# Kernel tuning notes

Measured on AMD Instinct MI355X. Metric: run time of the kernel, lower is better.

Reference implementation:

```python
import jax, jax.numpy as jnp
import numpy as np

B, S, H = 32, 1024, 512  # batch, src_len, hidden_dim


def setup_inputs() -> dict:
    key = jax.random.key(0)
    k1, k2, k3, k4, k5 = jax.random.split(key, 5)
    hidden = jax.random.normal(k1, (B, H), dtype=jnp.float32)
    encoder_outputs = jax.random.normal(k2, (B, S, 2 * H), dtype=jnp.float32)
    # nn.Linear(3H, H): weight stored here as [3H, H] (input-major) with bias [H]
    W = jax.random.normal(k3, (3 * H, H), dtype=jnp.float32) / np.sqrt(3 * H)
    b = jax.random.normal(k4, (H,), dtype=jnp.float32) * 0.01
    v = jax.random.normal(k5, (H,), dtype=jnp.float32) / np.sqrt(H)
    return {"hidden": hidden, "encoder_outputs": encoder_outputs, "W": W, "b": b, "v": v}


def reference(hidden, encoder_outputs, W, b, v):
    # concat((repeat(hidden), encoder_outputs)) @ W  ==  hidden @ W[:H] (broadcast) + enc @ W[H:]
    Wh, We = W[:H], W[H:]                         # [H,H], [2H,H]
    h_proj = hidden @ Wh                           # [B,H]
    e_proj = jnp.einsum('bse,eh->bsh', encoder_outputs, We)  # [B,S,H]
    energy = jnp.tanh(h_proj[:, None, :] + e_proj + b)       # [B,S,H]
    # bmm(v[B,1,H], energy^T[B,H,S]) -> scores [B,S]
    scores = jnp.einsum('bsh,h->bs', energy, v)
    return jax.nn.softmax(scores, axis=1)
```

## Files before the change

### kernel.cpp

```cpp
#include <hip/hip_runtime.h>
#include <math.h>

#define B_ 32
#define S_ 1024
#define H_ 512
#define K_ 1024
#define M_ (B_ * S_)

typedef __attribute__((ext_vector_type(8))) short bf16x8;
typedef __attribute__((ext_vector_type(4))) float f32x4;

__device__ __forceinline__ void split_bf16(float f, unsigned short& hi, unsigned short& lo) {
    unsigned u = __float_as_uint(f);
    unsigned rh = (u + 0x7fffu + ((u >> 16) & 1u)) >> 16;
    hi = (unsigned short)rh;
    float fh = __uint_as_float(rh << 16);
    float r = f - fh;
    unsigned ur = __float_as_uint(r);
    unsigned rl = (ur + 0x7fffu + ((ur >> 16) & 1u)) >> 16;
    lo = (unsigned short)rl;
}

__device__ __forceinline__ void split8_store(const float4& x, const float4& y,
                                             unsigned short* hiP, unsigned short* loP) {
    union { unsigned short us[8]; uint4 u; } h, l;
    split_bf16(x.x, h.us[0], l.us[0]);
    split_bf16(x.y, h.us[1], l.us[1]);
    split_bf16(x.z, h.us[2], l.us[2]);
    split_bf16(x.w, h.us[3], l.us[3]);
    split_bf16(y.x, h.us[4], l.us[4]);
    split_bf16(y.y, h.us[5], l.us[5]);
    split_bf16(y.z, h.us[6], l.us[6]);
    split_bf16(y.w, h.us[7], l.us[7]);
    *reinterpret_cast<uint4*>(hiP) = h.u;
    *reinterpret_cast<uint4*>(loP) = l.u;
}

__device__ __forceinline__ void async_copy16(const void* g, void* l) {
    __builtin_amdgcn_global_load_lds(
        (const __attribute__((address_space(1))) void*)g,
        (__attribute__((address_space(3))) void*)l, 16, 0, 0);
}

__global__ __launch_bounds__(256) void prep_kernel(
    const float* __restrict__ hidden, const float* __restrict__ W,
    const float* __restrict__ bias, float* __restrict__ hb,
    unsigned short* __restrict__ Wh, unsigned short* __restrict__ Wl)
{
    __shared__ float red[4][64];
    __shared__ float t[32][33];
    const int bx = blockIdx.x;
    if (bx < 256) {
        const int tid = threadIdx.x;
        const int h0  = (bx & 7) * 64;
        const int b   = bx >> 3;
        const int h   = h0 + (tid & 63);
        const int ks  = tid >> 6;
        const float* hrow = hidden + b * H_;
        float acc = 0.f;
        #pragma unroll 8
        for (int k = ks * 128; k < ks * 128 + 128; ++k)
            acc = fmaf(hrow[k], W[(size_t)k * H_ + h], acc);
        red[ks][tid & 63] = acc;
        __syncthreads();
        if (tid < 64)
            hb[b * H_ + h0 + tid] = red[0][tid] + red[1][tid] + red[2][tid]
                                  + red[3][tid] + bias[h0 + tid];
    } else {
        const float* We = W + (size_t)H_ * H_;
        const int cx = bx - 256;
        const int k0 = (cx & 31) * 32, n0 = (cx >> 5) * 32;
        const int tx = threadIdx.x & 31, ty = threadIdx.x >> 5;
        #pragma unroll
        for (int j = 0; j < 4; ++j) {
            const int k = ty + 8 * j;
            t[k][tx] = We[(size_t)(k0 + k) * H_ + n0 + tx];
        }
        __syncthreads();
        #pragma unroll
        for (int j = 0; j < 4; ++j) {
            const int n = ty + 8 * j;
            unsigned short hi, lo;
            split_bf16(t[tx][n], hi, lo);
            Wh[(size_t)(n0 + n) * K_ + k0 + tx] = hi;
            Wl[(size_t)(n0 + n) * K_ + k0 + tx] = lo;
        }
    }
}

__global__ __launch_bounds__(256, 2) void gemm_fused(
    const float* __restrict__ EO,
    const unsigned short* __restrict__ Bth,
    const unsigned short* __restrict__ Btl,
    const float* __restrict__ hb, const float* __restrict__ v,
    float* __restrict__ partial)
{
    __shared__ unsigned short ldsA[2][2][4096];
    __shared__ unsigned short ldsB[2][2][4096];

    const int tid  = threadIdx.x;
    const int nt   = blockIdx.x;
    const int mt   = blockIdx.y;
    const int row0 = mt * 128;
    const int col0 = nt * 128;
    const int batch = row0 >> 10;

    const int lane   = tid & 63;
    const int wave   = tid >> 6;
    const int wm     = wave >> 1, wn = wave & 1;
    const int lanelo = lane & 15, quad = lane >> 4;

    size_t gaA[2];
    int offA[2];
    #pragma unroll
    for (int s = 0; s < 2; ++s) {
        const int seg = tid + 256 * s;
        const int m = seg >> 2, sg = seg & 3;
        gaA[s] = (size_t)(row0 + m) * K_ + sg * 8;
        offA[s] = m * 32 + (sg ^ ((m >> 1) & 3)) * 8;
    }
    size_t gb[2];
    int offB[2];
    #pragma unroll
    for (int j = 0; j < 2; ++j) {
        const int iss = wave * 2 + j;
        const int r   = iss * 16 + (lane >> 2);
        const int qg  = (lane & 3) ^ ((r >> 1) & 3);
        gb[j] = (size_t)(col0 + r) * K_ + qg * 8;
        offB[j] = iss * 512;
    }

    f32x4 acc[4][4];
    #pragma unroll
    for (int i = 0; i < 4; ++i)
        #pragma unroll
        for (int j = 0; j < 4; ++j)
            acc[i][j] = (f32x4){0.f, 0.f, 0.f, 0.f};

    float4 a0[2], a1[2];
    #pragma unroll
    for (int s = 0; s < 2; ++s) {
        a0[s] = *reinterpret_cast<const float4*>(EO + gaA[s]);
        a1[s] = *reinterpret_cast<const float4*>(EO + gaA[s] + 4);
    }
    #pragma unroll
    for (int j = 0; j < 2; ++j) {
        async_copy16(Bth + gb[j], &ldsB[0][0][offB[j]]);
        async_copy16(Btl + gb[j], &ldsB[0][1][offB[j]]);
    }
    #pragma unroll
    for (int s = 0; s < 2; ++s)
        split8_store(a0[s], a1[s], &ldsA[0][0][offA[s]], &ldsA[0][1][offA[s]]);

    for (int i = 0; i < 32; ++i) {
        __syncthreads();
        const int cur = i & 1, nxt = cur ^ 1;
        const int k0n = 32 * (i + 1);
        if (i < 31) {
            #pragma unroll
            for (int s = 0; s < 2; ++s) {
                a0[s] = *reinterpret_cast<const float4*>(EO + gaA[s] + k0n);
                a1[s] = *reinterpret_cast<const float4*>(EO + gaA[s] + k0n + 4);
            }
            #pragma unroll
            for (int j = 0; j < 2; ++j) {
                async_copy16(Bth + gb[j] + k0n, &ldsB[nxt][0][offB[j]]);
                async_copy16(Btl + gb[j] + k0n, &ldsB[nxt][1][offB[j]]);
            }
        }

        bf16x8 a_h[4], a_l[4], b_h[4], b_l[4];
        #pragma unroll
        for (int fi = 0; fi < 4; ++fi) {
            const int m  = wm * 64 + fi * 16 + lanelo;
            const int sa = quad ^ ((m >> 1) & 3);
            a_h[fi] = *reinterpret_cast<const bf16x8*>(&ldsA[cur][0][m * 32 + sa * 8]);
            a_l[fi] = *reinterpret_cast<const bf16x8*>(&ldsA[cur][1][m * 32 + sa * 8]);
            const int n  = wn * 64 + fi * 16 + lanelo;
            const int sb = quad ^ ((n >> 1) & 3);
            b_h[fi] = *reinterpret_cast<const bf16x8*>(&ldsB[cur][0][n * 32 + sb * 8]);
            b_l[fi] = *reinterpret_cast<const bf16x8*>(&ldsB[cur][1][n * 32 + sb * 8]);
        }
        #pragma unroll
        for (int fi = 0; fi < 4; ++fi)
            #pragma unroll
            for (int fj = 0; fj < 4; ++fj) {
                acc[fi][fj] = __builtin_amdgcn_mfma_f32_16x16x32_bf16(
                    a_h[fi], b_h[fj], acc[fi][fj], 0, 0, 0);
                acc[fi][fj] = __builtin_amdgcn_mfma_f32_16x16x32_bf16(
                    a_h[fi], b_l[fj], acc[fi][fj], 0, 0, 0);
                acc[fi][fj] = __builtin_amdgcn_mfma_f32_16x16x32_bf16(
                    a_l[fi], b_h[fj], acc[fi][fj], 0, 0, 0);
            }

        if (i < 31) {
            #pragma unroll
            for (int s = 0; s < 2; ++s)
                split8_store(a0[s], a1[s],
                             &ldsA[nxt][0][offA[s]], &ldsA[nxt][1][offA[s]]);
        }
    }

    const float* hb_row = hb + batch * H_;
    float hbv[4], vv[4];
    #pragma unroll
    for (int fj = 0; fj < 4; ++fj) {
        const int c = col0 + wn * 64 + fj * 16 + lanelo;
        hbv[fj] = hb_row[c];
        vv[fj]  = v[c];
    }
    float* red = reinterpret_cast<float*>(&ldsA[0][0][0]);
    #pragma unroll
    for (int fi = 0; fi < 4; ++fi)
        #pragma unroll
        for (int r = 0; r < 4; ++r) {
            float rs = 0.f;
            #pragma unroll
            for (int fj = 0; fj < 4; ++fj)
                rs = fmaf(tanhf(acc[fi][fj][r] + hbv[fj]), vv[fj], rs);
            rs += __shfl_xor(rs, 1, 64);
            rs += __shfl_xor(rs, 2, 64);
            rs += __shfl_xor(rs, 4, 64);
            rs += __shfl_xor(rs, 8, 64);
            if (lanelo == 0) {
                const int row = wm * 64 + fi * 16 + quad * 4 + r;
                red[row * 2 + wn] = rs;
            }
        }
    __syncthreads();
    if (tid < 128)
        partial[(size_t)nt * M_ + row0 + tid] = red[tid * 2] + red[tid * 2 + 1];
}

__global__ __launch_bounds__(256) void softmax_kernel(
    const float* __restrict__ partial, float* __restrict__ out)
{
    const int b = blockIdx.x;
    const int tid = threadIdx.x;
    float val[4];
    float lmax = -3.0e38f;
    #pragma unroll
    for (int q = 0; q < 4; ++q) {
        const int idx = b * S_ + tid + 256 * q;
        float sum = partial[idx] + partial[M_ + idx] + partial[2 * M_ + idx] +
                    partial[3 * M_ + idx];
        val[q] = sum;
        lmax = fmaxf(lmax, sum);
    }
    #pragma unroll
    for (int off = 32; off > 0; off >>= 1)
        lmax = fmaxf(lmax, __shfl_down(lmax, off, 64));
    __shared__ float wmax[4];
    if ((tid & 63) == 0) wmax[tid >> 6] = lmax;
    __syncthreads();
    const float gmax = fmaxf(fmaxf(wmax[0], wmax[1]), fmaxf(wmax[2], wmax[3]));
    float lsum = 0.0f;
    #pragma unroll
    for (int q = 0; q < 4; ++q) {
        val[q] = expf(val[q] - gmax);
        lsum += val[q];
    }
    #pragma unroll
    for (int off = 32; off > 0; off >>= 1)
        lsum += __shfl_down(lsum, off, 64);
    __shared__ float wsum[4];
    if ((tid & 63) == 0) wsum[tid >> 6] = lsum;
    __syncthreads();
    const float inv = 1.0f / (wsum[0] + wsum[1] + wsum[2] + wsum[3]);
    #pragma unroll
    for (int q = 0; q < 4; ++q)
        out[b * S_ + tid + 256 * q] = val[q] * inv;
}

extern "C" void kernel_launch(void* const* d_in, const int* in_sizes, int n_in,
                              void* d_out, int out_size, void* d_ws, size_t ws_size,
                              hipStream_t stream) {
    const float* hidden = (const float*)d_in[0];
    const float* EO     = (const float*)d_in[1];
    const float* W      = (const float*)d_in[2];
    const float* bias   = (const float*)d_in[3];
    const float* v      = (const float*)d_in[4];
    float* out          = (float*)d_out;

    float* hb      = (float*)d_ws;
    float* partial = hb + B_ * H_;
    unsigned short* Wth = (unsigned short*)(partial + 4 * M_);
    unsigned short* Wtl = Wth + (size_t)H_ * K_;

    prep_kernel<<<768, 256, 0, stream>>>(hidden, W, bias, hb, Wth, Wtl);
    gemm_fused<<<dim3(4, M_ / 128), 256, 0, stream>>>(EO, Wth, Wtl, hb, v, partial);
    softmax_kernel<<<B_, 256, 0, stream>>>(partial, out);
}
```

Baseline: 317.1 us.

## Use 32x32x16 MFMA tiles, cheaper bf16 split, fast tanh, remap block order

The GEMM inner loop moves from 16x16x32 to 32x32x16 bf16 MFMA with 2x2 fragments per wave, which cuts LDS fragment reads per MFMA and raises work per instruction. The bf16 hi/lo split switches from round-to-nearest-even to a simpler add-0x8000 rounding packed with v_perm, reducing ALU work in the fp32-to-bf16 conversion. tanhf is replaced by an exp/rcp approximation, and a 1D grid is remapped so blocks are interleaved across M (an XCD/L2 locality swizzle). Risks are slight accuracy change from the approximate tanh and the rounding change, plus higher register pressure from the 16-wide accumulators.

```diff
diff --git a/kernel.cpp b/kernel.cpp
--- a/kernel.cpp
+++ b/kernel.cpp
@@ -8,32 +8,46 @@
 #define M_ (B_ * S_)
 
 typedef __attribute__((ext_vector_type(8))) short bf16x8;
-typedef __attribute__((ext_vector_type(4))) float f32x4;
+typedef __attribute__((ext_vector_type(16))) float f32x16;
 
 __device__ __forceinline__ void split_bf16(float f, unsigned short& hi, unsigned short& lo) {
     unsigned u = __float_as_uint(f);
-    unsigned rh = (u + 0x7fffu + ((u >> 16) & 1u)) >> 16;
-    hi = (unsigned short)rh;
-    float fh = __uint_as_float(rh << 16);
-    float r = f - fh;
-    unsigned ur = __float_as_uint(r);
-    unsigned rl = (ur + 0x7fffu + ((ur >> 16) & 1u)) >> 16;
-    lo = (unsigned short)rl;
+    unsigned r = u + 0x8000u;
+    hi = (unsigned short)(r >> 16);
+    float fh = __uint_as_float(r & 0xffff0000u);
+    float res = f - fh;
+    lo = (unsigned short)((__float_as_uint(res) + 0x8000u) >> 16);
 }
 
 __device__ __forceinline__ void split8_store(const float4& x, const float4& y,
                                              unsigned short* hiP, unsigned short* loP) {
-    union { unsigned short us[8]; uint4 u; } h, l;
-    split_bf16(x.x, h.us[0], l.us[0]);
-    split_bf16(x.y, h.us[1], l.us[1]);
-    split_bf16(x.z, h.us[2], l.us[2]);
-    split_bf16(x.w, h.us[3], l.us[3]);
-    split_bf16(y.x, h.us[4], l.us[4]);
-    split_bf16(y.y, h.us[5], l.us[5]);
-    split_bf16(y.z, h.us[6], l.us[6]);
-    split_bf16(y.w, h.us[7], l.us[7]);
-    *reinterpret_cast<uint4*>(hiP) = h.u;
-    *reinterpret_cast<uint4*>(loP) = l.u;
+    float f[8] = {x.x, x.y, x.z, x.w, y.x, y.y, y.z, y.w};
+    unsigned hr[8], lr[8];
+    #pragma unroll
+    for (int i = 0; i < 8; ++i) {
+        unsigned u = __float_as_uint(f[i]);
+        unsigned r = u + 0x8000u;
+        hr[i] = r;
+        float fh = __uint_as_float(r & 0xffff0000u);
+        lr[i] = __float_as_uint(f[i] - fh) + 0x8000u;
+    }
+    uint4 Hv, Lv;
+    Hv.x = __builtin_amdgcn_perm(hr[1], hr[0], 0x07060302u);
+    Hv.y = __builtin_amdgcn_perm(hr[3], hr[2], 0x07060302u);
+    Hv.z = __builtin_amdgcn_perm(hr[5], hr[4], 0x07060302u);
+    Hv.w = __builtin_amdgcn_perm(hr[7], hr[6], 0x07060302u);
+    Lv.x = __builtin_amdgcn_perm(lr[1], lr[0], 0x07060302u);
+    Lv.y = __builtin_amdgcn_perm(lr[3], lr[2], 0x07060302u);
+    Lv.z = __builtin_amdgcn_perm(lr[5], lr[4], 0x07060302u);
+    Lv.w = __builtin_amdgcn_perm(lr[7], lr[6], 0x07060302u);
+    *reinterpret_cast<uint4*>(hiP) = Hv;
+    *reinterpret_cast<uint4*>(loP) = Lv;
+}
+
+__device__ __forceinline__ float fast_tanh(float x) {
+    float xc = fminf(fmaxf(x, -15.f), 15.f);
+    float t = __expf(2.0f * xc);
+    return (t - 1.0f) * __builtin_amdgcn_rcpf(t + 1.0f);
 }
 
 __device__ __forceinline__ void async_copy16(const void* g, void* l) {
@@ -99,8 +113,10 @@
     __shared__ unsigned short ldsB[2][2][4096];
 
     const int tid  = threadIdx.x;
-    const int nt   = blockIdx.x;
-    const int mt   = blockIdx.y;
+    const int bid  = blockIdx.x;
+    const int j    = bid >> 3;
+    const int mt   = (bid & 7) * 32 + (j >> 2);
+    const int nt   = j & 3;
     const int row0 = mt * 128;
     const int col0 = nt * 128;
     const int batch = row0 >> 10;
@@ -108,7 +124,7 @@
     const int lane   = tid & 63;
     const int wave   = tid >> 6;
     const int wm     = wave >> 1, wn = wave & 1;
-    const int lanelo = lane & 15, quad = lane >> 4;
+    const int lane32 = lane & 31, khalf = lane >> 5;
 
     size_t gaA[2];
     int offA[2];
@@ -122,20 +138,22 @@
     size_t gb[2];
     int offB[2];
     #pragma unroll
-    for (int j = 0; j < 2; ++j) {
-        const int iss = wave * 2 + j;
+    for (int jj = 0; jj < 2; ++jj) {
+        const int iss = wave * 2 + jj;
         const int r   = iss * 16 + (lane >> 2);
         const int qg  = (lane & 3) ^ ((r >> 1) & 3);
-        gb[j] = (size_t)(col0 + r) * K_ + qg * 8;
-        offB[j] = iss * 512;
-    }
-
-    f32x4 acc[4][4];
-    #pragma unroll
-    for (int i = 0; i < 4; ++i)
-        #pragma unroll
-        for (int j = 0; j < 4; ++j)
-            acc[i][j] = (f32x4){0.f, 0.f, 0.f, 0.f};
+        gb[jj] = (size_t)(col0 + r) * K_ + qg * 8;
+        offB[jj] = iss * 512;
+    }
+
+    f32x16 acc[2][2];
+    #pragma unroll
+    for (int fi = 0; fi < 2; ++fi)
+        #pragma unroll
+        for (int fj = 0; fj < 2; ++fj)
+            #pragma unroll
+            for (int e = 0; e < 16; ++e)
+                acc[fi][fj][e] = 0.f;
 
     float4 a0[2], a1[2];
     #pragma unroll
@@ -144,9 +162,9 @@
         a1[s] = *reinterpret_cast<const float4*>(EO + gaA[s] + 4);
     }
     #pragma unroll
-    for (int j = 0; j < 2; ++j) {
-        async_copy16(Bth + gb[j], &ldsB[0][0][offB[j]]);
-        async_copy16(Btl + gb[j], &ldsB[0][1][offB[j]]);
+    for (int jj = 0; jj < 2; ++jj) {
+        async_copy16(Bth + gb[jj], &ldsB[0][0][offB[jj]]);
+        async_copy16(Btl + gb[jj], &ldsB[0][1][offB[jj]]);
     }
     #pragma unroll
     for (int s = 0; s < 2; ++s)
@@ -163,35 +181,48 @@
                 a1[s] = *reinterpret_cast<const float4*>(EO + gaA[s] + k0n + 4);
             }
             #pragma unroll
-            for (int j = 0; j < 2; ++j) {
-                async_copy16(Bth + gb[j] + k0n, &ldsB[nxt][0][offB[j]]);
-                async_copy16(Btl + gb[j] + k0n, &ldsB[nxt][1][offB[j]]);
-            }
-        }
-
-        bf16x8 a_h[4], a_l[4], b_h[4], b_l[4];
-        #pragma unroll
-        for (int fi = 0; fi < 4; ++fi) {
-            const int m  = wm * 64 + fi * 16 + lanelo;
-            const int sa = quad ^ ((m >> 1) & 3);
-            a_h[fi] = *reinterpret_cast<const bf16x8*>(&ldsA[cur][0][m * 32 + sa * 8]);
-            a_l[fi] = *reinterpret_cast<const bf16x8*>(&ldsA[cur][1][m * 32 + sa * 8]);
-            const int n  = wn * 64 + fi * 16 + lanelo;
-            const int sb = quad ^ ((n >> 1) & 3);
-            b_h[fi] = *reinterpret_cast<const bf16x8*>(&ldsB[cur][0][n * 32 + sb * 8]);
-            b_l[fi] = *reinterpret_cast<const bf16x8*>(&ldsB[cur][1][n * 32 + sb * 8]);
-        }
-        #pragma unroll
-        for (int fi = 0; fi < 4; ++fi)
-            #pragma unroll
-            for (int fj = 0; fj < 4; ++fj) {
-                acc[fi][fj] = __builtin_amdgcn_mfma_f32_16x16x32_bf16(
-                    a_h[fi], b_h[fj], acc[fi][fj], 0, 0, 0);
-                acc[fi][fj] = __builtin_amdgcn_mfma_f32_16x16x32_bf16(
-                    a_h[fi], b_l[fj], acc[fi][fj], 0, 0, 0);
-                acc[fi][fj] = __builtin_amdgcn_mfma_f32_16x16x32_bf16(
-                    a_l[fi], b_h[fj], acc[fi][fj], 0, 0, 0);
-            }
+            for (int jj = 0; jj < 2; ++jj) {
+                async_copy16(Bth + gb[jj] + k0n, &ldsB[nxt][0][offB[jj]]);
+                async_copy16(Btl + gb[jj] + k0n, &ldsB[nxt][1][offB[jj]]);
+            }
+        }
+
+        bf16x8 a_h[2][2], a_l[2][2], b_h[2][2], b_l[2][2];
+        #pragma unroll
+        for (int fi = 0; fi < 2; ++fi) {
+            const int m   = wm * 64 + fi * 32 + lane32;
+            const int swz = (m >> 1) & 3;
+            #pragma unroll
+            for (int ks = 0; ks < 2; ++ks) {
+                const int sa = (ks * 2 + khalf) ^ swz;
+                a_h[fi][ks] = *reinterpret_cast<const bf16x8*>(&ldsA[cur][0][m * 32 + sa * 8]);
+                a_l[fi][ks] = *reinterpret_cast<const bf16x8*>(&ldsA[cur][1][m * 32 + sa * 8]);
+            }
+        }
+        #pragma unroll
+        for (int fj = 0; fj < 2; ++fj) {
+            const int n   = wn * 64 + fj * 32 + lane32;
+            const int swz = (n >> 1) & 3;
+            #pragma unroll
+            for (int ks = 0; ks < 2; ++ks) {
+                const int sb = (ks * 2 + khalf) ^ swz;
+                b_h[fj][ks] = *reinterpret_cast<const bf16x8*>(&ldsB[cur][0][n * 32 + sb * 8]);
+                b_l[fj][ks] = *reinterpret_cast<const bf16x8*>(&ldsB[cur][1][n * 32 + sb * 8]);
+            }
+        }
+        #pragma unroll
+        for (int fi = 0; fi < 2; ++fi)
+            #pragma unroll
+            for (int fj = 0; fj < 2; ++fj)
+                #pragma unroll
+                for (int ks = 0; ks < 2; ++ks) {
+                    acc[fi][fj] = __builtin_amdgcn_mfma_f32_32x32x16_bf16(
+                        a_h[fi][ks], b_h[fj][ks], acc[fi][fj], 0, 0, 0);
+                    acc[fi][fj] = __builtin_amdgcn_mfma_f32_32x32x16_bf16(
+                        a_h[fi][ks], b_l[fj][ks], acc[fi][fj], 0, 0, 0);
+                    acc[fi][fj] = __builtin_amdgcn_mfma_f32_32x32x16_bf16(
+                        a_l[fi][ks], b_h[fj][ks], acc[fi][fj], 0, 0, 0);
+                }
 
         if (i < 31) {
             #pragma unroll
@@ -202,28 +233,29 @@
     }
 
     const float* hb_row = hb + batch * H_;
-    float hbv[4], vv[4];
-    #pragma unroll
-    for (int fj = 0; fj < 4; ++fj) {
-        const int c = col0 + wn * 64 + fj * 16 + lanelo;
+    float hbv[2], vv[2];
+    #pragma unroll
+    for (int fj = 0; fj < 2; ++fj) {
+        const int c = col0 + wn * 64 + fj * 32 + lane32;
         hbv[fj] = hb_row[c];
         vv[fj]  = v[c];
     }
     float* red = reinterpret_cast<float*>(&ldsA[0][0][0]);
     #pragma unroll
-    for (int fi = 0; fi < 4; ++fi)
-        #pragma unroll
-        for (int r = 0; r < 4; ++r) {
+    for (int fi = 0; fi < 2; ++fi)
+        #pragma unroll
+        for (int r = 0; r < 16; ++r) {
             float rs = 0.f;
             #pragma unroll
-            for (int fj = 0; fj < 4; ++fj)
-                rs = fmaf(tanhf(acc[fi][fj][r] + hbv[fj]), vv[fj], rs);
+            for (int fj = 0; fj < 2; ++fj)
+                rs = fmaf(fast_tanh(acc[fi][fj][r] + hbv[fj]), vv[fj], rs);
             rs += __shfl_xor(rs, 1, 64);
             rs += __shfl_xor(rs, 2, 64);
             rs += __shfl_xor(rs, 4, 64);
             rs += __shfl_xor(rs, 8, 64);
-            if (lanelo == 0) {
-                const int row = wm * 64 + fi * 16 + quad * 4 + r;
+            rs += __shfl_xor(rs, 16, 64);
+            if (lane32 == 0) {
+                const int row = wm * 64 + fi * 32 + (r & 3) + 8 * (r >> 2) + 4 * khalf;
                 red[row * 2 + wn] = rs;
             }
         }
@@ -288,6 +320,6 @@
     unsigned short* Wtl = Wth + (size_t)H_ * K_;
 
     prep_kernel<<<768, 256, 0, stream>>>(hidden, W, bias, hb, Wth, Wtl);
-    gemm_fused<<<dim3(4, M_ / 128), 256, 0, stream>>>(EO, Wth, Wtl, hb, v, partial);
+    gemm_fused<<<dim3(1024), 256, 0, stream>>>(EO, Wth, Wtl, hb, v, partial);
     softmax_kernel<<<B_, 256, 0, stream>>>(partial, out);
 }
```

Result: no change. 320.2 us (+1.0%).
